# Kernel optimization log

Hardware: AMD Instinct MI355X
Metric: run time of the kernel (lower is better)

The kernel has to match this reference:

```python
import jax, jax.numpy as jnp
import numpy as np

D_MODEL = 1024
NHEAD = 16
HEAD_DIM = D_MODEL // NHEAD
EPS = 1e-5


def layer_norm(x, gamma, beta):
    mu = jnp.mean(x, axis=-1, keepdims=True)
    var = jnp.mean(jnp.square(x - mu), axis=-1, keepdims=True)
    return (x - mu) * jax.lax.rsqrt(var + EPS) * gamma + beta


def setup_inputs() -> dict:
    key = jax.random.key(0)
    ks = jax.random.split(key, 12)
    d = D_MODEL
    s = 1.0 / np.sqrt(d)
    return {
        "x": jax.random.normal(ks[0], (4, 2048, d), dtype=jnp.float32),
        "wq": jax.random.normal(ks[1], (d, d), dtype=jnp.float32) * s,
        "wk": jax.random.normal(ks[2], (d, d), dtype=jnp.float32) * s,
        "wv": jax.random.normal(ks[3], (d, d), dtype=jnp.float32) * s,
        "wo": jax.random.normal(ks[4], (d, d), dtype=jnp.float32) * s,
        "bo": jnp.zeros((d,), dtype=jnp.float32),
        "gx": jnp.ones((d,), dtype=jnp.float32),
        "bx": jnp.zeros((d,), dtype=jnp.float32),
        "gf": jnp.ones((d,), dtype=jnp.float32),
        "bf": jnp.zeros((d,), dtype=jnp.float32),
        "w1": jax.random.normal(ks[5], (d, d), dtype=jnp.float32) * s,
        "b1": jnp.zeros((d,), dtype=jnp.float32),
        "w2": jax.random.normal(ks[6], (d, d), dtype=jnp.float32) * s,
        "b2": jnp.zeros((d,), dtype=jnp.float32),
    }


def reference(x, wq, wk, wv, wo, bo, gx, bx, gf, bf, w1, b1, w2, b2):
    B, S, D = x.shape
    H, Dh = NHEAD, HEAD_DIM
    xs = layer_norm(x, gx, bx)
    q = (xs @ wq).reshape(B, S, H, Dh)
    k = (xs @ wk).reshape(B, S, H, Dh)
    v = (xs @ wv).reshape(B, S, H, Dh)
    scores = jnp.einsum("bqhd,bkhd->bhqk", q, k) / jnp.sqrt(jnp.float32(Dh))
    attn = jax.nn.softmax(scores, axis=-1)  # dropout p=0 -> identity
    o = jnp.einsum("bhqk,bkhd->bqhd", attn, v).reshape(B, S, D)
    attn_out = o @ wo + bo
    xt = x + attn_out
    h = layer_norm(xt, gf, bf)
    ffn = jax.nn.relu(h @ w1 + b1) @ w2 + b2
    return xt + ffn
```

## Files before the change

### kernel.cpp

```cpp
#include <hip/hip_runtime.h>
#include <hip/hip_bf16.h>

typedef __bf16 bf16;
typedef bf16 bf16x8 __attribute__((ext_vector_type(8)));
typedef bf16 bf16x4 __attribute__((ext_vector_type(4)));
typedef float f32x4 __attribute__((ext_vector_type(4)));
typedef float f32x16 __attribute__((ext_vector_type(16)));

#define AS1 __attribute__((address_space(1)))
#define AS3 __attribute__((address_space(3)))

static constexpr int SEQ = 2048;
static constexpr int NH  = 16;
static constexpr int DH  = 64;
static constexpr float SCLQ = 0.125f * 1.44269504088896340736f;

__device__ __forceinline__ void gload16(const void* g, void* l) {
  __builtin_amdgcn_global_load_lds((const AS1 void*)g, (AS3 void*)l, 16, 0, 0);
}

__device__ __forceinline__ unsigned pk2(float a, float b) {
  union { bf16 h[2]; unsigned u; } z;
  z.h[0] = (bf16)a; z.h[1] = (bf16)b;
  return z.u;
}

__device__ __forceinline__ void plswap(unsigned &a, unsigned &b) {
  asm volatile("v_permlane32_swap_b32 %0, %1" : "+v"(a), "+v"(b));
}

#define MFMA32(d, a, b) d = __builtin_amdgcn_mfma_f32_32x32x16_bf16(a, b, d, 0, 0, 0)

__global__ __launch_bounds__(256) void prep_w(
    const float* __restrict__ w0, const float* __restrict__ w1,
    const float* __restrict__ w2, const float* __restrict__ w3,
    const float* __restrict__ w4, const float* __restrict__ w5,
    bf16* __restrict__ dst)
{
  __shared__ float tile[64][65];
  int bid = blockIdx.x;
  int wi = bid >> 8;
  int tl = bid & 255;
  int tk = (tl >> 4) << 6;
  int tn = (tl & 15) << 6;
  const float* W = w0;
  if (wi == 1) W = w1; else if (wi == 2) W = w2; else if (wi == 3) W = w3;
  else if (wi == 4) W = w4; else if (wi == 5) W = w5;
  int t = threadIdx.x;
  #pragma unroll
  for (int rep = 0; rep < 16; ++rep) {
    int idx = rep * 256 + t;
    int i = idx >> 6, j = idx & 63;
    tile[i][j] = W[(size_t)(tk + i) * 1024 + tn + j];
  }
  __syncthreads();
  bf16* out = dst + (size_t)wi * 1024 * 1024;
  #pragma unroll
  for (int rep = 0; rep < 16; ++rep) {
    int idx = rep * 256 + t;
    int i = idx >> 6, j = idx & 63;
    out[(size_t)(tn + i) * 1024 + tk + j] = (bf16)tile[j][i];
  }
}

__global__ __launch_bounds__(256) void ln_k(
    const float* __restrict__ x, const float* __restrict__ g,
    const float* __restrict__ bb, bf16* __restrict__ out)
{
  int row = blockIdx.x;
  int t = threadIdx.x;
  float4 v = ((const float4*)(x + (size_t)row * 1024))[t];
  float s  = v.x + v.y + v.z + v.w;
  float s2 = v.x * v.x + v.y * v.y + v.z * v.z + v.w * v.w;
  #pragma unroll
  for (int m = 1; m < 64; m <<= 1) { s += __shfl_xor(s, m); s2 += __shfl_xor(s2, m); }
  __shared__ float red[8];
  int w = t >> 6;
  if ((t & 63) == 0) { red[w] = s; red[4 + w] = s2; }
  __syncthreads();
  s  = red[0] + red[1] + red[2] + red[3];
  s2 = red[4] + red[5] + red[6] + red[7];
  float mu  = s * (1.0f / 1024.0f);
  float var = s2 * (1.0f / 1024.0f) - mu * mu;
  float rst = rsqrtf(var + 1e-5f);
  float4 gv = ((const float4*)g)[t];
  float4 bv = ((const float4*)bb)[t];
  bf16x4 o;
  o[0] = (bf16)((v.x - mu) * rst * gv.x + bv.x);
  o[1] = (bf16)((v.y - mu) * rst * gv.y + bv.y);
  o[2] = (bf16)((v.z - mu) * rst * gv.z + bv.z);
  o[3] = (bf16)((v.w - mu) * rst * gv.w + bv.w);
  *(bf16x4*)(out + (size_t)row * 1024 + t * 4) = o;
}

template<int EPI, int NT>
__global__ __launch_bounds__(256) void gemm_k(
    const bf16* __restrict__ A, const bf16* __restrict__ Bt,
    const float* __restrict__ bias, const float* __restrict__ res,
    float* __restrict__ outf, bf16* __restrict__ outb)
{
  __shared__ bf16 lA[128 * 64];
  __shared__ bf16 lB[128 * 64];
  int t = threadIdx.x;
  int wg = blockIdx.x;
  int swz = (wg & 7) * (NT * 8) + (wg >> 3);
  int mt = swz / NT, nt = swz % NT;
  int lane = t & 63, w = t >> 6;
  int l16 = lane & 15, lh = lane >> 4;
  int wr = w >> 1, wc = w & 1;

  f32x4 acc[4][4] = {};
  const size_t mbase = (size_t)mt * 128;
  const size_t nbase = (size_t)nt * 128;
  int u = t & 7;

  for (int ks = 0; ks < 16; ++ks) {
    int k0 = ks * 64;
    #pragma unroll
    for (int i = 0; i < 4; ++i) {
      int row = i * 32 + (t >> 3);
      int up = u ^ (row & 7);
      gload16(A  + (mbase + row) * 1024 + k0 + up * 8, lA + i * 2048 + w * 512);
      gload16(Bt + (nbase + row) * 1024 + k0 + up * 8, lB + i * 2048 + w * 512);
    }
    __syncthreads();
    #pragma unroll
    for (int kc = 0; kc < 2; ++kc) {
      bf16x8 af[4], bfr[4];
      #pragma unroll
      for (int mi = 0; mi < 4; ++mi) {
        int row = wr * 64 + mi * 16 + l16;
        af[mi] = *(const bf16x8*)(lA + row * 64 + (((kc * 4 + lh) ^ (row & 7)) * 8));
      }
      #pragma unroll
      for (int ni = 0; ni < 4; ++ni) {
        int row = wc * 64 + ni * 16 + l16;
        bfr[ni] = *(const bf16x8*)(lB + row * 64 + (((kc * 4 + lh) ^ (row & 7)) * 8));
      }
      #pragma unroll
      for (int mi = 0; mi < 4; ++mi)
        #pragma unroll
        for (int ni = 0; ni < 4; ++ni)
          acc[mi][ni] = __builtin_amdgcn_mfma_f32_16x16x32_bf16(af[mi], bfr[ni], acc[mi][ni], 0, 0, 0);
    }
    __syncthreads();
  }

  int mrow0 = mt * 128 + wr * 64;
  int ncol0 = nt * 128 + wc * 64;
  #pragma unroll
  for (int mi = 0; mi < 4; ++mi) {
    #pragma unroll
    for (int ni = 0; ni < 4; ++ni) {
      if constexpr (EPI == 0) {
        int gcol = ncol0 + ni * 16 + l16;
        int which = gcol >> 10;
        int col = gcol & 1023;
        int h = col >> 6, dh = col & 63;
        bf16* dst = outb + (size_t)which * (size_t)(4 * NH * SEQ * DH);
        if (which == 2) {
          int s0 = mrow0 + mi * 16 + lh * 4;
          int b = s0 >> 11, s = s0 & 2047;
          bf16x4 pkv;
          #pragma unroll
          for (int r = 0; r < 4; ++r) pkv[r] = (bf16)acc[mi][ni][r];
          *(bf16x4*)(dst + (((size_t)((b * NH + h) * DH + dh)) << 11) + s) = pkv;
        } else {
          #pragma unroll
          for (int r = 0; r < 4; ++r) {
            int grow = mrow0 + mi * 16 + lh * 4 + r;
            int b = grow >> 11, s = grow & 2047;
            float v = acc[mi][ni][r];
            if (which == 0) v *= SCLQ;
            dst[(((size_t)((b * NH + h) * SEQ + s)) << 6) + dh] = (bf16)v;
          }
        }
      } else {
        #pragma unroll
        for (int r = 0; r < 4; ++r) {
          int grow = mrow0 + mi * 16 + lh * 4 + r;
          int gcol = ncol0 + ni * 16 + l16;
          float v = acc[mi][ni][r];
          if constexpr (EPI == 2) {
            size_t idx = (size_t)grow * 1024 + gcol;
            outf[idx] = v + bias[gcol] + res[idx];
          } else {
            size_t idx = (size_t)grow * 1024 + gcol;
            float z = v + bias[gcol];
            outb[idx] = (bf16)(z > 0.f ? z : 0.f);
          }
        }
      }
    }
  }
}

__global__ __launch_bounds__(256, 2) void attn_k(
    const bf16* __restrict__ q, const bf16* __restrict__ kk,
    const bf16* __restrict__ vt, bf16* __restrict__ o)
{
  __shared__ bf16 lK[2][4096];
  __shared__ bf16 lV[2][4096];

  int t = threadIdx.x;
  int lane = t & 63, w = t >> 6;
  int l31 = lane & 31, hi = lane >> 5;
  int bid = blockIdx.x;
  int swz = (bid & 7) * 64 + (bid >> 3);
  int bh = swz >> 3, qt = swz & 7;
  int q0 = qt * 256 + w * 64;
  size_t bhS = (size_t)bh * SEQ;

  const bf16* qrow0 = q + (bhS + q0 + l31) * 64 + hi * 8;
  const bf16* qrow1 = qrow0 + 32 * 64;
  bf16x8 aq0[4], aq1[4];
  #pragma unroll
  for (int ks = 0; ks < 4; ++ks) {
    aq0[ks] = *(const bf16x8*)(qrow0 + ks * 16);
    aq1[ks] = *(const bf16x8*)(qrow1 + ks * 16);
  }

  int srow = t >> 3;
  int u8 = (t & 7) ^ (srow & 7);
  const bf16* kSrc = kk + (bhS + srow) * 64 + u8 * 8;
  const bf16* vSrc = vt + ((size_t)bh * 64 + srow) * SEQ + u8 * 8;

  f32x16 oa00 = {}, oa01 = {}, oa10 = {}, oa11 = {};
  float lsum0 = 0.f, lsum1 = 0.f;

  gload16(kSrc,            &lK[0][w * 512]);
  gload16(kSrc + 2048,     &lK[0][2048 + w * 512]);
  gload16(vSrc,            &lV[0][w * 512]);
  gload16(vSrc + 32 * SEQ, &lV[0][2048 + w * 512]);
  __syncthreads();

  #pragma unroll 2
  for (int kt = 0; kt < 32; ++kt) {
    const int cur = kt & 1;
    if (kt < 31) {
      const bf16* ks2 = kSrc + (size_t)(kt + 1) * 4096;
      const bf16* vs2 = vSrc + (kt + 1) * 64;
      gload16(ks2,            &lK[cur ^ 1][w * 512]);
      gload16(ks2 + 2048,     &lK[cur ^ 1][2048 + w * 512]);
      gload16(vs2,            &lV[cur ^ 1][w * 512]);
      gload16(vs2 + 32 * SEQ, &lV[cur ^ 1][2048 + w * 512]);
    }

    const bf16* bK = &lK[cur][0];
    const bf16* bV = &lV[cur][0];

    f32x16 sA0 = {}, sB0 = {}, sA1 = {}, sB1 = {};
    __builtin_amdgcn_s_setprio(1);
    #pragma unroll
    for (int ks = 0; ks < 4; ++ks) {
      int u = ((2 * ks + hi) ^ (l31 & 7)) * 8;
      bf16x8 k0 = *(const bf16x8*)(bK + l31 * 64 + u);
      bf16x8 k1 = *(const bf16x8*)(bK + (32 + l31) * 64 + u);
      MFMA32(sA0, k0, aq0[ks]);
      MFMA32(sA1, k0, aq1[ks]);
      MFMA32(sB0, k1, aq0[ks]);
      MFMA32(sB1, k1, aq1[ks]);
    }
    __builtin_amdgcn_s_setprio(0);

    unsigned cv0[4][4], cv1[4][4];
    {
      float p[32];
      #pragma unroll
      for (int i = 0; i < 16; ++i) {
        p[i]      = __builtin_amdgcn_exp2f(sA0[i]);
        p[16 + i] = __builtin_amdgcn_exp2f(sB0[i]);
      }
      float t8[8];
      #pragma unroll
      for (int i = 0; i < 8; ++i)
        t8[i] = (p[4 * i] + p[4 * i + 1]) + (p[4 * i + 2] + p[4 * i + 3]);
      lsum0 += ((t8[0] + t8[1]) + (t8[2] + t8[3])) + ((t8[4] + t8[5]) + (t8[6] + t8[7]));
      #pragma unroll
      for (int ks = 0; ks < 4; ++ks) {
        int g = 8 * ks;
        unsigned X0 = pk2(p[g],     p[g + 1]), X1 = pk2(p[g + 2], p[g + 3]);
        unsigned Y0 = pk2(p[g + 4], p[g + 5]), Y1 = pk2(p[g + 6], p[g + 7]);
        plswap(X0, Y0);
        plswap(X1, Y1);
        cv0[ks][0] = X0; cv0[ks][1] = X1; cv0[ks][2] = Y0; cv0[ks][3] = Y1;
      }
    }
    {
      float p[32];
      #pragma unroll
      for (int i = 0; i < 16; ++i) {
        p[i]      = __builtin_amdgcn_exp2f(sA1[i]);
        p[16 + i] = __builtin_amdgcn_exp2f(sB1[i]);
      }
      float t8[8];
      #pragma unroll
      for (int i = 0; i < 8; ++i)
        t8[i] = (p[4 * i] + p[4 * i + 1]) + (p[4 * i + 2] + p[4 * i + 3]);
      lsum1 += ((t8[0] + t8[1]) + (t8[2] + t8[3])) + ((t8[4] + t8[5]) + (t8[6] + t8[7]));
      #pragma unroll
      for (int ks = 0; ks < 4; ++ks) {
        int g = 8 * ks;
        unsigned X0 = pk2(p[g],     p[g + 1]), X1 = pk2(p[g + 2], p[g + 3]);
        unsigned Y0 = pk2(p[g + 4], p[g + 5]), Y1 = pk2(p[g + 6], p[g + 7]);
        plswap(X0, Y0);
        plswap(X1, Y1);
        cv1[ks][0] = X0; cv1[ks][1] = X1; cv1[ks][2] = Y0; cv1[ks][3] = Y1;
      }
    }

    __builtin_amdgcn_s_setprio(1);
    #pragma unroll
    for (int ks = 0; ks < 4; ++ks) {
      int u = ((2 * ks + hi) ^ (l31 & 7)) * 8;
      bf16x8 v0 = *(const bf16x8*)(bV + l31 * 64 + u);
      bf16x8 v1 = *(const bf16x8*)(bV + (32 + l31) * 64 + u);
      union { unsigned u[4]; bf16x8 v; } a0, a1;
      a0.u[0] = cv0[ks][0]; a0.u[1] = cv0[ks][1]; a0.u[2] = cv0[ks][2]; a0.u[3] = cv0[ks][3];
      a1.u[0] = cv1[ks][0]; a1.u[1] = cv1[ks][1]; a1.u[2] = cv1[ks][2]; a1.u[3] = cv1[ks][3];
      MFMA32(oa00, a0.v, v0);
      MFMA32(oa01, a0.v, v1);
      MFMA32(oa10, a1.v, v0);
      MFMA32(oa11, a1.v, v1);
    }
    __builtin_amdgcn_s_setprio(0);

    __syncthreads();
  }

  lsum0 += __shfl_xor(lsum0, 32);
  lsum1 += __shfl_xor(lsum1, 32);
  float inv0 = 1.0f / lsum0;
  float inv1 = 1.0f / lsum1;
  int bb = bh >> 4, hh = bh & 15;
  size_t obase = ((size_t)bb * SEQ + q0) * 1024 + (size_t)hh * 64;
  #pragma unroll
  for (int r = 0; r < 16; ++r) {
    int qrw = (r & 3) + 8 * (r >> 2) + 4 * hi;
    float iv0 = __shfl(inv0, qrw);
    float iv1 = __shfl(inv1, qrw);
    size_t b0 = obase + (size_t)qrw * 1024;
    size_t b1 = obase + (size_t)(32 + qrw) * 1024;
    o[b0 + l31]      = (bf16)(oa00[r] * iv0);
    o[b0 + 32 + l31] = (bf16)(oa01[r] * iv0);
    o[b1 + l31]      = (bf16)(oa10[r] * iv1);
    o[b1 + 32 + l31] = (bf16)(oa11[r] * iv1);
  }
}

extern "C" void kernel_launch(void* const* d_in, const int* in_sizes, int n_in,
                              void* d_out, int out_size, void* d_ws, size_t ws_size,
                              hipStream_t stream) {
  const float* x   = (const float*)d_in[0];
  const float* wq  = (const float*)d_in[1];
  const float* wk  = (const float*)d_in[2];
  const float* wv  = (const float*)d_in[3];
  const float* wo  = (const float*)d_in[4];
  const float* bo  = (const float*)d_in[5];
  const float* gx  = (const float*)d_in[6];
  const float* bx  = (const float*)d_in[7];
  const float* gf  = (const float*)d_in[8];
  const float* bfp = (const float*)d_in[9];
  const float* w1  = (const float*)d_in[10];
  const float* b1  = (const float*)d_in[11];
  const float* w2  = (const float*)d_in[12];
  const float* b2  = (const float*)d_in[13];

  char* ws = (char*)d_ws;
  const size_t MB = 1024 * 1024;
  bf16*  wT  = (bf16*)ws;
  bf16*  xs  = (bf16*)(ws + 12 * MB);
  bf16*  qb  = (bf16*)(ws + 28 * MB);
  bf16*  kb  = (bf16*)(ws + 44 * MB);
  bf16*  vtb = (bf16*)(ws + 60 * MB);
  bf16*  ob  = (bf16*)(ws + 12 * MB);
  float* xt  = (float*)(ws + 28 * MB);
  bf16*  hb  = (bf16*)(ws + 60 * MB);
  bf16*  a1  = (bf16*)(ws + 12 * MB);
  float* out = (float*)d_out;

  prep_w<<<1536, 256, 0, stream>>>(wq, wk, wv, wo, w1, w2, wT);
  ln_k<<<8192, 256, 0, stream>>>(x, gx, bx, xs);
  gemm_k<0, 24><<<1536, 256, 0, stream>>>(xs, wT, nullptr, nullptr, nullptr, qb);
  attn_k<<<512, 256, 0, stream>>>(qb, kb, vtb, ob);
  gemm_k<2, 8><<<512, 256, 0, stream>>>(ob, wT + (size_t)3 * MB, bo, x, xt, nullptr);
  ln_k<<<8192, 256, 0, stream>>>(xt, gf, bfp, hb);
  gemm_k<3, 8><<<512, 256, 0, stream>>>(hb, wT + (size_t)4 * MB, b1, nullptr, nullptr, a1);
  gemm_k<2, 8><<<512, 256, 0, stream>>>(a1, wT + (size_t)5 * MB, b2, xt, out, nullptr);
}
```

Before: 270.4 us.

## Software-pipeline attention so P·V of previous tile overlaps current exp

Restructures the attention key loop into a software pipeline: each iteration computes QK^T for tile t while issuing the P·V MFMAs for tile t-1 interleaved with the exp/pack of tile t. V LDS buffers grow from two to four so the previous tile's V stays resident, and packed probabilities are double-buffered in registers. This targets the serialization between exp (VALU) and MFMA work, but raises register and LDS pressure, which could hurt occupancy at the declared two blocks per CU.

```diff
diff --git a/kernel.cpp b/kernel.cpp
--- a/kernel.cpp
+++ b/kernel.cpp
@@ -200,7 +200,7 @@
     const bf16* __restrict__ vt, bf16* __restrict__ o)
 {
   __shared__ bf16 lK[2][4096];
-  __shared__ bf16 lV[2][4096];
+  __shared__ bf16 lV[4][4096];
 
   int t = threadIdx.x;
   int lane = t & 63, w = t >> 6;
@@ -227,6 +227,7 @@
 
   f32x16 oa00 = {}, oa01 = {}, oa10 = {}, oa11 = {};
   float lsum0 = 0.f, lsum1 = 0.f;
+  unsigned cvA0[4][4], cvA1[4][4], cvB0[4][4], cvB1[4][4];
 
   gload16(kSrc,            &lK[0][w * 512]);
   gload16(kSrc + 2048,     &lK[0][2048 + w * 512]);
@@ -234,98 +235,91 @@
   gload16(vSrc + 32 * SEQ, &lV[0][2048 + w * 512]);
   __syncthreads();
 
-  #pragma unroll 2
-  for (int kt = 0; kt < 32; ++kt) {
-    const int cur = kt & 1;
-    if (kt < 31) {
-      const bf16* ks2 = kSrc + (size_t)(kt + 1) * 4096;
-      const bf16* vs2 = vSrc + (kt + 1) * 64;
-      gload16(ks2,            &lK[cur ^ 1][w * 512]);
-      gload16(ks2 + 2048,     &lK[cur ^ 1][2048 + w * 512]);
-      gload16(vs2,            &lV[cur ^ 1][w * 512]);
-      gload16(vs2 + 32 * SEQ, &lV[cur ^ 1][2048 + w * 512]);
-    }
-
-    const bf16* bK = &lK[cur][0];
-    const bf16* bV = &lV[cur][0];
-
-    f32x16 sA0 = {}, sB0 = {}, sA1 = {}, sB1 = {};
+#define ATTN_ITER(T, CVO0, CVO1, CVN0, CVN1, PREF, PV)                        \
+  do {                                                                        \
+    const int T_ = (T);                                                       \
+    const bf16* bK  = &lK[T_ & 1][0];                                         \
+    const bf16* bVp = &lV[(T_ - 1) & 3][0];                                   \
+    if (PREF) {                                                               \
+      bf16* nK = &lK[(T_ + 1) & 1][0];                                        \
+      bf16* nV = &lV[(T_ + 1) & 3][0];                                        \
+      const bf16* ks2 = kSrc + (size_t)(T_ + 1) * 4096;                       \
+      const bf16* vs2 = vSrc + (T_ + 1) * 64;                                 \
+      gload16(ks2,            nK + w * 512);                                  \
+      gload16(ks2 + 2048,     nK + 2048 + w * 512);                           \
+      gload16(vs2,            nV + w * 512);                                  \
+      gload16(vs2 + 32 * SEQ, nV + 2048 + w * 512);                           \
+    }                                                                         \
+    f32x16 sA0 = {}, sB0 = {}, sA1 = {}, sB1 = {};                            \
+    __builtin_amdgcn_s_setprio(1);                                            \
+    _Pragma("unroll")                                                         \
+    for (int ks = 0; ks < 4; ++ks) {                                          \
+      int u = ((2 * ks + hi) ^ (l31 & 7)) * 8;                                \
+      bf16x8 k0 = *(const bf16x8*)(bK + l31 * 64 + u);                        \
+      bf16x8 k1 = *(const bf16x8*)(bK + (32 + l31) * 64 + u);                 \
+      MFMA32(sA0, k0, aq0[ks]); MFMA32(sA1, k0, aq1[ks]);                     \
+      MFMA32(sB0, k1, aq0[ks]); MFMA32(sB1, k1, aq1[ks]);                     \
+    }                                                                         \
+    __builtin_amdgcn_s_setprio(0);                                            \
+    _Pragma("unroll")                                                         \
+    for (int ks = 0; ks < 4; ++ks) {                                          \
+      if (PV) {                                                               \
+        int u = ((2 * ks + hi) ^ (l31 & 7)) * 8;                              \
+        bf16x8 v0 = *(const bf16x8*)(bVp + l31 * 64 + u);                     \
+        bf16x8 v1 = *(const bf16x8*)(bVp + (32 + l31) * 64 + u);              \
+        union { unsigned u4[4]; bf16x8 v; } a0, a1;                           \
+        a0.u4[0] = CVO0[ks][0]; a0.u4[1] = CVO0[ks][1];                       \
+        a0.u4[2] = CVO0[ks][2]; a0.u4[3] = CVO0[ks][3];                       \
+        a1.u4[0] = CVO1[ks][0]; a1.u4[1] = CVO1[ks][1];                       \
+        a1.u4[2] = CVO1[ks][2]; a1.u4[3] = CVO1[ks][3];                       \
+        MFMA32(oa00, a0.v, v0); MFMA32(oa01, a0.v, v1);                       \
+        MFMA32(oa10, a1.v, v0); MFMA32(oa11, a1.v, v1);                       \
+      }                                                                       \
+      float e0[8], e1[8];                                                     \
+      _Pragma("unroll")                                                       \
+      for (int j = 0; j < 8; ++j) {                                           \
+        e0[j] = __builtin_amdgcn_exp2f((ks < 2 ? sA0 : sB0)[(ks & 1) * 8 + j]); \
+        e1[j] = __builtin_amdgcn_exp2f((ks < 2 ? sA1 : sB1)[(ks & 1) * 8 + j]); \
+      }                                                                       \
+      lsum0 += ((e0[0] + e0[1]) + (e0[2] + e0[3])) + ((e0[4] + e0[5]) + (e0[6] + e0[7])); \
+      lsum1 += ((e1[0] + e1[1]) + (e1[2] + e1[3])) + ((e1[4] + e1[5]) + (e1[6] + e1[7])); \
+      unsigned X0 = pk2(e0[0], e0[1]), X1 = pk2(e0[2], e0[3]);                \
+      unsigned Y0 = pk2(e0[4], e0[5]), Y1 = pk2(e0[6], e0[7]);                \
+      plswap(X0, Y0); plswap(X1, Y1);                                         \
+      CVN0[ks][0] = X0; CVN0[ks][1] = X1; CVN0[ks][2] = Y0; CVN0[ks][3] = Y1; \
+      unsigned Z0 = pk2(e1[0], e1[1]), Z1 = pk2(e1[2], e1[3]);                \
+      unsigned W0 = pk2(e1[4], e1[5]), W1 = pk2(e1[6], e1[7]);                \
+      plswap(Z0, W0); plswap(Z1, W1);                                         \
+      CVN1[ks][0] = Z0; CVN1[ks][1] = Z1; CVN1[ks][2] = W0; CVN1[ks][3] = W1; \
+    }                                                                         \
+    __syncthreads();                                                          \
+  } while (0)
+
+  ATTN_ITER(0, cvB0, cvB1, cvA0, cvA1, true, false);
+  for (int kt = 1; kt < 31; kt += 2) {
+    ATTN_ITER(kt,     cvA0, cvA1, cvB0, cvB1, true, true);
+    ATTN_ITER(kt + 1, cvB0, cvB1, cvA0, cvA1, true, true);
+  }
+  ATTN_ITER(31, cvA0, cvA1, cvB0, cvB1, false, true);
+#undef ATTN_ITER
+
+  {
+    const bf16* bVp = &lV[3][0];
     __builtin_amdgcn_s_setprio(1);
     #pragma unroll
     for (int ks = 0; ks < 4; ++ks) {
       int u = ((2 * ks + hi) ^ (l31 & 7)) * 8;
-      bf16x8 k0 = *(const bf16x8*)(bK + l31 * 64 + u);
-      bf16x8 k1 = *(const bf16x8*)(bK + (32 + l31) * 64 + u);
-      MFMA32(sA0, k0, aq0[ks]);
-      MFMA32(sA1, k0, aq1[ks]);
-      MFMA32(sB0, k1, aq0[ks]);
-      MFMA32(sB1, k1, aq1[ks]);
+      bf16x8 v0 = *(const bf16x8*)(bVp + l31 * 64 + u);
+      bf16x8 v1 = *(const bf16x8*)(bVp + (32 + l31) * 64 + u);
+      union { unsigned u4[4]; bf16x8 v; } a0, a1;
+      a0.u4[0] = cvB0[ks][0]; a0.u4[1] = cvB0[ks][1];
+      a0.u4[2] = cvB0[ks][2]; a0.u4[3] = cvB0[ks][3];
+      a1.u4[0] = cvB1[ks][0]; a1.u4[1] = cvB1[ks][1];
+      a1.u4[2] = cvB1[ks][2]; a1.u4[3] = cvB1[ks][3];
+      MFMA32(oa00, a0.v, v0); MFMA32(oa01, a0.v, v1);
+      MFMA32(oa10, a1.v, v0); MFMA32(oa11, a1.v, v1);
     }
     __builtin_amdgcn_s_setprio(0);
-
-    unsigned cv0[4][4], cv1[4][4];
-    {
-      float p[32];
-      #pragma unroll
-      for (int i = 0; i < 16; ++i) {
-        p[i]      = __builtin_amdgcn_exp2f(sA0[i]);
-        p[16 + i] = __builtin_amdgcn_exp2f(sB0[i]);
-      }
-      float t8[8];
-      #pragma unroll
-      for (int i = 0; i < 8; ++i)
-        t8[i] = (p[4 * i] + p[4 * i + 1]) + (p[4 * i + 2] + p[4 * i + 3]);
-      lsum0 += ((t8[0] + t8[1]) + (t8[2] + t8[3])) + ((t8[4] + t8[5]) + (t8[6] + t8[7]));
-      #pragma unroll
-      for (int ks = 0; ks < 4; ++ks) {
-        int g = 8 * ks;
-        unsigned X0 = pk2(p[g],     p[g + 1]), X1 = pk2(p[g + 2], p[g + 3]);
-        unsigned Y0 = pk2(p[g + 4], p[g + 5]), Y1 = pk2(p[g + 6], p[g + 7]);
-        plswap(X0, Y0);
-        plswap(X1, Y1);
-        cv0[ks][0] = X0; cv0[ks][1] = X1; cv0[ks][2] = Y0; cv0[ks][3] = Y1;
-      }
-    }
-    {
-      float p[32];
-      #pragma unroll
-      for (int i = 0; i < 16; ++i) {
-        p[i]      = __builtin_amdgcn_exp2f(sA1[i]);
-        p[16 + i] = __builtin_amdgcn_exp2f(sB1[i]);
-      }
-      float t8[8];
-      #pragma unroll
-      for (int i = 0; i < 8; ++i)
-        t8[i] = (p[4 * i] + p[4 * i + 1]) + (p[4 * i + 2] + p[4 * i + 3]);
-      lsum1 += ((t8[0] + t8[1]) + (t8[2] + t8[3])) + ((t8[4] + t8[5]) + (t8[6] + t8[7]));
-      #pragma unroll
-      for (int ks = 0; ks < 4; ++ks) {
-        int g = 8 * ks;
-        unsigned X0 = pk2(p[g],     p[g + 1]), X1 = pk2(p[g + 2], p[g + 3]);
-        unsigned Y0 = pk2(p[g + 4], p[g + 5]), Y1 = pk2(p[g + 6], p[g + 7]);
-        plswap(X0, Y0);
-        plswap(X1, Y1);
-        cv1[ks][0] = X0; cv1[ks][1] = X1; cv1[ks][2] = Y0; cv1[ks][3] = Y1;
-      }
-    }
-
-    __builtin_amdgcn_s_setprio(1);
-    #pragma unroll
-    for (int ks = 0; ks < 4; ++ks) {
-      int u = ((2 * ks + hi) ^ (l31 & 7)) * 8;
-      bf16x8 v0 = *(const bf16x8*)(bV + l31 * 64 + u);
-      bf16x8 v1 = *(const bf16x8*)(bV + (32 + l31) * 64 + u);
-      union { unsigned u[4]; bf16x8 v; } a0, a1;
-      a0.u[0] = cv0[ks][0]; a0.u[1] = cv0[ks][1]; a0.u[2] = cv0[ks][2]; a0.u[3] = cv0[ks][3];
-      a1.u[0] = cv1[ks][0]; a1.u[1] = cv1[ks][1]; a1.u[2] = cv1[ks][2]; a1.u[3] = cv1[ks][3];
-      MFMA32(oa00, a0.v, v0);
-      MFMA32(oa01, a0.v, v1);
-      MFMA32(oa10, a1.v, v0);
-      MFMA32(oa11, a1.v, v1);
-    }
-    __builtin_amdgcn_s_setprio(0);
-
-    __syncthreads();
   }
 
   lsum0 += __shfl_xor(lsum0, 32);
```

New measurement: 270.8 us. About the same (+0.1%).

## Shrink attention blocks to two waves and double the grid

Applied to the files above, without the earlier changes.

The attention kernel now uses 128-thread blocks covering 128 query rows instead of 256, with 1024 blocks instead of 512. Each wave loads four K/V chunks per stage rather than one, so each block still stages full 64-row tiles. The goal is better CU load balance across the 256 CUs and more independent blocks in flight. The cost is that each K/V tile is fetched into LDS twice as often overall, and the swizzled block-to-head mapping changes.

```diff
diff --git a/kernel.cpp b/kernel.cpp
--- a/kernel.cpp
+++ b/kernel.cpp
@@ -195,7 +195,7 @@
   }
 }
 
-__global__ __launch_bounds__(256, 2) void attn_k(
+__global__ __launch_bounds__(128, 2) void attn_k(
     const bf16* __restrict__ q, const bf16* __restrict__ kk,
     const bf16* __restrict__ vt, bf16* __restrict__ o)
 {
@@ -206,9 +206,9 @@
   int lane = t & 63, w = t >> 6;
   int l31 = lane & 31, hi = lane >> 5;
   int bid = blockIdx.x;
-  int swz = (bid & 7) * 64 + (bid >> 3);
-  int bh = swz >> 3, qt = swz & 7;
-  int q0 = qt * 256 + w * 64;
+  int swz = (bid & 7) * 128 + (bid >> 3);
+  int bh = swz >> 4, qt = swz & 15;
+  int q0 = qt * 128 + w * 64;
   size_t bhS = (size_t)bh * SEQ;
 
   const bf16* qrow0 = q + (bhS + q0 + l31) * 64 + hi * 8;
@@ -220,31 +220,32 @@
     aq1[ks] = *(const bf16x8*)(qrow1 + ks * 16);
   }
 
-  int srow = t >> 3;
-  int u8 = (t & 7) ^ (srow & 7);
-  const bf16* kSrc = kk + (bhS + srow) * 64 + u8 * 8;
-  const bf16* vSrc = vt + ((size_t)bh * 64 + srow) * SEQ + u8 * 8;
+  int lrow = lane >> 3;
+  int usw  = (lane & 7) ^ lrow;
+  const bf16* kSrc = kk + (bhS + w * 32 + lrow) * 64 + usw * 8;
+  const bf16* vSrc = vt + ((size_t)bh * 64 + w * 32 + lrow) * SEQ + usw * 8;
+
+#define STAGE(BUF, T)                                                         \
+  do {                                                                        \
+    const bf16* ks_ = kSrc + (size_t)(T) * 4096;                              \
+    const bf16* vs_ = vSrc + (T) * 64;                                        \
+    _Pragma("unroll")                                                         \
+    for (int c = 0; c < 4; ++c) {                                             \
+      gload16(ks_ + c * 512,     &lK[BUF][w * 2048 + c * 512]);               \
+      gload16(vs_ + c * 8 * SEQ, &lV[BUF][w * 2048 + c * 512]);               \
+    }                                                                         \
+  } while (0)
 
   f32x16 oa00 = {}, oa01 = {}, oa10 = {}, oa11 = {};
   float lsum0 = 0.f, lsum1 = 0.f;
 
-  gload16(kSrc,            &lK[0][w * 512]);
-  gload16(kSrc + 2048,     &lK[0][2048 + w * 512]);
-  gload16(vSrc,            &lV[0][w * 512]);
-  gload16(vSrc + 32 * SEQ, &lV[0][2048 + w * 512]);
+  STAGE(0, 0);
   __syncthreads();
 
   #pragma unroll 2
   for (int kt = 0; kt < 32; ++kt) {
     const int cur = kt & 1;
-    if (kt < 31) {
-      const bf16* ks2 = kSrc + (size_t)(kt + 1) * 4096;
-      const bf16* vs2 = vSrc + (kt + 1) * 64;
-      gload16(ks2,            &lK[cur ^ 1][w * 512]);
-      gload16(ks2 + 2048,     &lK[cur ^ 1][2048 + w * 512]);
-      gload16(vs2,            &lV[cur ^ 1][w * 512]);
-      gload16(vs2 + 32 * SEQ, &lV[cur ^ 1][2048 + w * 512]);
-    }
+    if (kt < 31) STAGE(cur ^ 1, kt + 1);
 
     const bf16* bK = &lK[cur][0];
     const bf16* bV = &lV[cur][0];
@@ -315,9 +316,9 @@
       int u = ((2 * ks + hi) ^ (l31 & 7)) * 8;
       bf16x8 v0 = *(const bf16x8*)(bV + l31 * 64 + u);
       bf16x8 v1 = *(const bf16x8*)(bV + (32 + l31) * 64 + u);
-      union { unsigned u[4]; bf16x8 v; } a0, a1;
-      a0.u[0] = cv0[ks][0]; a0.u[1] = cv0[ks][1]; a0.u[2] = cv0[ks][2]; a0.u[3] = cv0[ks][3];
-      a1.u[0] = cv1[ks][0]; a1.u[1] = cv1[ks][1]; a1.u[2] = cv1[ks][2]; a1.u[3] = cv1[ks][3];
+      union { unsigned u4[4]; bf16x8 v; } a0, a1;
+      a0.u4[0] = cv0[ks][0]; a0.u4[1] = cv0[ks][1]; a0.u4[2] = cv0[ks][2]; a0.u4[3] = cv0[ks][3];
+      a1.u4[0] = cv1[ks][0]; a1.u4[1] = cv1[ks][1]; a1.u4[2] = cv1[ks][2]; a1.u4[3] = cv1[ks][3];
       MFMA32(oa00, a0.v, v0);
       MFMA32(oa01, a0.v, v1);
       MFMA32(oa10, a1.v, v0);
@@ -327,6 +328,7 @@
 
     __syncthreads();
   }
+#undef STAGE
 
   lsum0 += __shfl_xor(lsum0, 32);
   lsum1 += __shfl_xor(lsum1, 32);
@@ -382,7 +384,7 @@
   prep_w<<<1536, 256, 0, stream>>>(wq, wk, wv, wo, w1, w2, wT);
   ln_k<<<8192, 256, 0, stream>>>(x, gx, bx, xs);
   gemm_k<0, 24><<<1536, 256, 0, stream>>>(xs, wT, nullptr, nullptr, nullptr, qb);
-  attn_k<<<512, 256, 0, stream>>>(qb, kb, vtb, ob);
+  attn_k<<<1024, 128, 0, stream>>>(qb, kb, vtb, ob);
   gemm_k<2, 8><<<512, 256, 0, stream>>>(ob, wT + (size_t)3 * MB, bo, x, xt, nullptr);
   ln_k<<<8192, 256, 0, stream>>>(xt, gf, bfp, hb);
   gemm_k<3, 8><<<512, 256, 0, stream>>>(hb, wT + (size_t)4 * MB, b1, nullptr, nullptr, a1);
```

Measured after the change: 278.1 us. 1.03x slower.

## Split attention over two key halves and merge partials in a combine kernel

Applied to the files above, without the earlier changes.

The attention kernel now splits each query tile's key/value range into two halves, which doubles the grid from 512 to 1024 blocks. The launch-bounds occupancy hint rises from 2 to 4. Each half writes unnormalized partial outputs (fp32 for one half, bf16 for the other) plus its row sums. A new elementwise combine kernel adds the two halves and normalizes. The goal is better CU fill on a grid that previously gave only about two blocks per CU. The cost is an extra launch and roughly 100 MB of additional global traffic for partials, and the merge relies on softmax exponentials sharing a common reference across halves.

```diff
diff --git a/kernel.cpp b/kernel.cpp
--- a/kernel.cpp
+++ b/kernel.cpp
@@ -195,9 +195,11 @@
   }
 }
 
-__global__ __launch_bounds__(256, 2) void attn_k(
+__global__ __launch_bounds__(256, 4) void attn_k(
     const bf16* __restrict__ q, const bf16* __restrict__ kk,
-    const bf16* __restrict__ vt, bf16* __restrict__ o)
+    const bf16* __restrict__ vt,
+    float* __restrict__ pA, bf16* __restrict__ pB,
+    float* __restrict__ lsA, float* __restrict__ lsB)
 {
   __shared__ bf16 lK[2][4096];
   __shared__ bf16 lV[2][4096];
@@ -206,8 +208,10 @@
   int lane = t & 63, w = t >> 6;
   int l31 = lane & 31, hi = lane >> 5;
   int bid = blockIdx.x;
-  int swz = (bid & 7) * 64 + (bid >> 3);
-  int bh = swz >> 3, qt = swz & 7;
+  int swz = (bid & 7) * 128 + (bid >> 3);
+  int half = swz & 1;
+  int rest = swz >> 1;
+  int bh = rest >> 3, qt = rest & 7;
   int q0 = qt * 256 + w * 64;
   size_t bhS = (size_t)bh * SEQ;
 
@@ -222,8 +226,8 @@
 
   int srow = t >> 3;
   int u8 = (t & 7) ^ (srow & 7);
-  const bf16* kSrc = kk + (bhS + srow) * 64 + u8 * 8;
-  const bf16* vSrc = vt + ((size_t)bh * 64 + srow) * SEQ + u8 * 8;
+  const bf16* kSrc = kk + (bhS + half * 1024 + srow) * 64 + u8 * 8;
+  const bf16* vSrc = vt + ((size_t)bh * 64 + srow) * SEQ + half * 1024 + u8 * 8;
 
   f32x16 oa00 = {}, oa01 = {}, oa10 = {}, oa11 = {};
   float lsum0 = 0.f, lsum1 = 0.f;
@@ -235,9 +239,9 @@
   __syncthreads();
 
   #pragma unroll 2
-  for (int kt = 0; kt < 32; ++kt) {
+  for (int kt = 0; kt < 16; ++kt) {
     const int cur = kt & 1;
-    if (kt < 31) {
+    if (kt < 15) {
       const bf16* ks2 = kSrc + (size_t)(kt + 1) * 4096;
       const bf16* vs2 = vSrc + (kt + 1) * 64;
       gload16(ks2,            &lK[cur ^ 1][w * 512]);
@@ -315,9 +319,9 @@
       int u = ((2 * ks + hi) ^ (l31 & 7)) * 8;
       bf16x8 v0 = *(const bf16x8*)(bV + l31 * 64 + u);
       bf16x8 v1 = *(const bf16x8*)(bV + (32 + l31) * 64 + u);
-      union { unsigned u[4]; bf16x8 v; } a0, a1;
-      a0.u[0] = cv0[ks][0]; a0.u[1] = cv0[ks][1]; a0.u[2] = cv0[ks][2]; a0.u[3] = cv0[ks][3];
-      a1.u[0] = cv1[ks][0]; a1.u[1] = cv1[ks][1]; a1.u[2] = cv1[ks][2]; a1.u[3] = cv1[ks][3];
+      union { unsigned u4[4]; bf16x8 v; } a0, a1;
+      a0.u4[0] = cv0[ks][0]; a0.u4[1] = cv0[ks][1]; a0.u4[2] = cv0[ks][2]; a0.u4[3] = cv0[ks][3];
+      a1.u4[0] = cv1[ks][0]; a1.u4[1] = cv1[ks][1]; a1.u4[2] = cv1[ks][2]; a1.u4[3] = cv1[ks][3];
       MFMA32(oa00, a0.v, v0);
       MFMA32(oa01, a0.v, v1);
       MFMA32(oa10, a1.v, v0);
@@ -330,22 +334,52 @@
 
   lsum0 += __shfl_xor(lsum0, 32);
   lsum1 += __shfl_xor(lsum1, 32);
-  float inv0 = 1.0f / lsum0;
-  float inv1 = 1.0f / lsum1;
+  float* ls = half ? lsB : lsA;
+  if (hi == 0) {
+    ls[bh * 2048 + q0 + l31]      = lsum0;
+    ls[bh * 2048 + q0 + 32 + l31] = lsum1;
+  }
   int bb = bh >> 4, hh = bh & 15;
   size_t obase = ((size_t)bb * SEQ + q0) * 1024 + (size_t)hh * 64;
   #pragma unroll
   for (int r = 0; r < 16; ++r) {
     int qrw = (r & 3) + 8 * (r >> 2) + 4 * hi;
-    float iv0 = __shfl(inv0, qrw);
-    float iv1 = __shfl(inv1, qrw);
     size_t b0 = obase + (size_t)qrw * 1024;
     size_t b1 = obase + (size_t)(32 + qrw) * 1024;
-    o[b0 + l31]      = (bf16)(oa00[r] * iv0);
-    o[b0 + 32 + l31] = (bf16)(oa01[r] * iv0);
-    o[b1 + l31]      = (bf16)(oa10[r] * iv1);
-    o[b1 + 32 + l31] = (bf16)(oa11[r] * iv1);
-  }
+    if (half == 0) {
+      pA[b0 + l31]      = oa00[r];
+      pA[b0 + 32 + l31] = oa01[r];
+      pA[b1 + l31]      = oa10[r];
+      pA[b1 + 32 + l31] = oa11[r];
+    } else {
+      pB[b0 + l31]      = (bf16)oa00[r];
+      pB[b0 + 32 + l31] = (bf16)oa01[r];
+      pB[b1 + l31]      = (bf16)oa10[r];
+      pB[b1 + 32 + l31] = (bf16)oa11[r];
+    }
+  }
+}
+
+__global__ __launch_bounds__(256) void attn_combine(
+    const float* __restrict__ pA, const bf16* __restrict__ pBr,
+    const float* __restrict__ lsA, const float* __restrict__ lsB,
+    bf16* __restrict__ ob)
+{
+  size_t c = (size_t)blockIdx.x * 256 + threadIdx.x;
+  size_t i = c * 4;
+  int b = (int)(i >> 21);
+  int s = (int)((i >> 10) & 2047);
+  int h = (int)((i >> 6) & 15);
+  int li = (b * 16 + h) * 2048 + s;
+  float inv = 1.0f / (lsA[li] + lsB[li]);
+  float4 a = *(const float4*)(pA + i);
+  bf16x4 bq = *(const bf16x4*)(pBr + i);
+  bf16x4 o;
+  o[0] = (bf16)((a.x + (float)bq[0]) * inv);
+  o[1] = (bf16)((a.y + (float)bq[1]) * inv);
+  o[2] = (bf16)((a.z + (float)bq[2]) * inv);
+  o[3] = (bf16)((a.w + (float)bq[3]) * inv);
+  *(bf16x4*)(ob + i) = o;
 }
 
 extern "C" void kernel_launch(void* const* d_in, const int* in_sizes, int n_in,
@@ -373,6 +407,10 @@
   bf16*  qb  = (bf16*)(ws + 28 * MB);
   bf16*  kb  = (bf16*)(ws + 44 * MB);
   bf16*  vtb = (bf16*)(ws + 60 * MB);
+  float* pA  = (float*)d_out;
+  bf16*  pB  = (bf16*)(ws + 12 * MB);
+  float* lsA = (float*)ws;
+  float* lsB = (float*)(ws + 524288);
   bf16*  ob  = (bf16*)(ws + 12 * MB);
   float* xt  = (float*)(ws + 28 * MB);
   bf16*  hb  = (bf16*)(ws + 60 * MB);
@@ -382,7 +420,8 @@
   prep_w<<<1536, 256, 0, stream>>>(wq, wk, wv, wo, w1, w2, wT);
   ln_k<<<8192, 256, 0, stream>>>(x, gx, bx, xs);
   gemm_k<0, 24><<<1536, 256, 0, stream>>>(xs, wT, nullptr, nullptr, nullptr, qb);
-  attn_k<<<512, 256, 0, stream>>>(qb, kb, vtb, ob);
+  attn_k<<<1024, 256, 0, stream>>>(qb, kb, vtb, pA, pB, lsA, lsB);
+  attn_combine<<<8192, 256, 0, stream>>>(pA, pB, lsA, lsB, ob);
   gemm_k<2, 8><<<512, 256, 0, stream>>>(ob, wT + (size_t)3 * MB, bo, x, xt, nullptr);
   ln_k<<<8192, 256, 0, stream>>>(xt, gf, bfp, hb);
   gemm_k<3, 8><<<512, 256, 0, stream>>>(hb, wT + (size_t)4 * MB, b1, nullptr, nullptr, a1);
```

Measured after the change: 676.3 us. 150% more time.
